# Optimization experiments

Measured on AMD Instinct MI355X. Metric: run time of the kernel, lower is better.

## Reference

```python
import jax, jax.numpy as jnp
import numpy as np

B, CIN, COUT = 2, 64, 64
D, H, W = 8, 32, 32
KD = KH = KW = 3
K = KD * KH * KW  # 27
STRIDE, PAD, DIL = 1, 1, 1
DOUT = (D + 2 * PAD - DIL * (KD - 1) - 1) // STRIDE + 1
HOUT = (H + 2 * PAD - DIL * (KH - 1) - 1) // STRIDE + 1
WOUT = (W + 2 * PAD - DIL * (KW - 1) - 1) // STRIDE + 1


def setup_inputs() -> dict:
    key = jax.random.key(0)
    k1, k2, k3, k4 = jax.random.split(key, 4)
    x = jax.random.normal(k1, (B, CIN, D, H, W), dtype=jnp.float32)
    offset = jax.random.normal(k2, (B, 3 * K, DOUT, HOUT, WOUT), dtype=jnp.float32)
    weight = jax.random.normal(k3, (COUT, CIN, KD, KH, KW), dtype=jnp.float32) * 0.05
    bias = jax.random.normal(k4, (COUT,), dtype=jnp.float32) * 0.1
    return {"x": x, "offset": offset, "weight": weight, "bias": bias}


def _trilinear_sample(xb, zd, zh, zw):
    # xb: [C, D, H, W]; zd/zh/zw: [K, P] float sampling coords (zero padding outside)
    Dd, Hh, Ww = xb.shape[1], xb.shape[2], xb.shape[3]
    d0 = jnp.floor(zd); h0 = jnp.floor(zh); w0 = jnp.floor(zw)
    fd = zd - d0; fh = zh - h0; fw = zw - w0
    d0i = d0.astype(jnp.int32); h0i = h0.astype(jnp.int32); w0i = w0.astype(jnp.int32)
    acc = jnp.zeros((xb.shape[0],) + zd.shape, dtype=xb.dtype)
    for dd in (0, 1):
        for dh in (0, 1):
            for dw in (0, 1):
                di = d0i + dd; hi = h0i + dh; wi = w0i + dw
                wgt = ((fd if dd else 1.0 - fd) * (fh if dh else 1.0 - fh)
                       * (fw if dw else 1.0 - fw))
                valid = ((di >= 0) & (di < Dd) & (hi >= 0) & (hi < Hh)
                         & (wi >= 0) & (wi < Ww)).astype(xb.dtype)
                v = xb[:, jnp.clip(di, 0, Dd - 1), jnp.clip(hi, 0, Hh - 1),
                       jnp.clip(wi, 0, Ww - 1)]  # [C, K, P]
                acc = acc + v * (wgt * valid)[None]
    return acc


def _deform_conv3d(x, offset, weight, bias):
    Bb = x.shape[0]
    P = DOUT * HOUT * WOUT
    # kernel taps
    kd, kh, kw = jnp.unravel_index(jnp.arange(K), (KD, KH, KW))
    # output grid
    od, oh, ow = jnp.meshgrid(jnp.arange(DOUT), jnp.arange(HOUT), jnp.arange(WOUT), indexing="ij")
    base_d = (od[None] * STRIDE - PAD + kd[:, None, None, None] * DIL).astype(jnp.float32)  # [K,Do,Ho,Wo]
    base_h = (oh[None] * STRIDE - PAD + kh[:, None, None, None] * DIL).astype(jnp.float32)
    base_w = (ow[None] * STRIDE - PAD + kw[:, None, None, None] * DIL).astype(jnp.float32)
    off = offset.reshape(Bb, K, 3, DOUT, HOUT, WOUT)  # per-tap (dd, dh, dw)
    zd = (base_d[None] + off[:, :, 0]).reshape(Bb, K, P)
    zh = (base_h[None] + off[:, :, 1]).reshape(Bb, K, P)
    zw = (base_w[None] + off[:, :, 2]).reshape(Bb, K, P)
    sampled = jax.vmap(_trilinear_sample)(x, zd, zh, zw)  # [B, C, K, P]
    wmat = weight.reshape(COUT, CIN, K)
    out = jnp.einsum("bckp,ock->bop", sampled, wmat)  # [B, COUT, P]
    out = out + bias[None, :, None]
    return out.reshape(Bb, COUT, DOUT, HOUT, WOUT)


def reference(x, offset, weight, bias):
    return _deform_conv3d(x, offset, weight, bias)
```

## Files before the change

kernel.cpp:

```cpp
#include <hip/hip_runtime.h>
#include <hip/hip_bf16.h>


#define BB    2
#define CINC  64
#define COUTC 64
#define DDEP  8
#define HGT   32
#define WID   32
#define KK    27
#define KGRP  3
#define KPG   9
#define KPH   3
#define PP    8192
#define TP    64
#define LDW   72

typedef short s16x8 __attribute__((ext_vector_type(8)));
typedef float f32x4 __attribute__((ext_vector_type(4)));

__device__ __forceinline__ unsigned short f2bf(float f) {
    unsigned u = __builtin_bit_cast(unsigned, f);
    u += 0x7FFFu + ((u >> 16) & 1u);
    return (unsigned short)(u >> 16);
}

__device__ __forceinline__ unsigned pack2bf(float lo, float hi) {
    return (unsigned)f2bf(lo) | ((unsigned)f2bf(hi) << 16);
}

__device__ __forceinline__ float bfu_lo(unsigned v) {
    return __builtin_bit_cast(float, v << 16);
}
__device__ __forceinline__ float bfu_hi(unsigned v) {
    return __builtin_bit_cast(float, v & 0xFFFF0000u);
}

__global__ void pre_kernel(const float* __restrict__ x, const float* __restrict__ w,
                           unsigned short* __restrict__ xt, unsigned short* __restrict__ wt) {
    __shared__ float sT[64][65];
    const int t    = threadIdx.x;
    const int lane = t & 63;
    const int wv   = t >> 6;
    const int half = lane >> 5;
    const int c2   = lane & 31;
    int blk = blockIdx.x;
    if (blk < 256) {
        int b  = blk >> 7;
        int s0 = (blk & 127) * 64;
        #pragma unroll
        for (int i = 0; i < 16; ++i) {
            int c = wv * 16 + i;
            sT[c][lane] = x[(size_t)(b * CINC + c) * PP + s0 + lane];
        }
        __syncthreads();
        #pragma unroll
        for (int i = 0; i < 8; ++i) {
            int s = wv * 16 + 2 * i + half;
            unsigned pk = pack2bf(sT[2 * c2][s], sT[2 * c2 + 1][s]);
            *(unsigned*)&xt[(size_t)(b * PP + s0 + s) * 64 + 2 * c2] = pk;
        }
    } else {
        int id = (blk - 256) * 256 + t;
        if (id < KK * COUTC * CINC) {
            int c = id & 63;
            int o = (id >> 6) & 63;
            int k = id >> 12;
            wt[id] = f2bf(w[(o * CINC + c) * KK + k]);
        }
    }
}

__global__ __launch_bounds__(256, 3) void deform_kernel(
    const unsigned short* __restrict__ xt, const float* __restrict__ off,
    const unsigned short* __restrict__ wt, const float* __restrict__ bias,
    float* __restrict__ out)
{
    __shared__ unsigned short sW[KPH * COUTC * LDW] __attribute__((aligned(16)));
    __shared__ unsigned short sS[TP * LDW]          __attribute__((aligned(16)));
    __shared__ int   sIdx[KPH][TP][8] __attribute__((aligned(16)));
    __shared__ float sCf[KPH][TP][8]  __attribute__((aligned(16)));

    const int t    = threadIdx.x;
    const int lane = t & 63;
    const int wv   = t >> 6;
    const int half = lane >> 5;
    const int c2   = lane & 31;
    const int b    = blockIdx.x >> 7;
    const int p0   = (blockIdx.x & 127) * TP;
    const int kg   = blockIdx.y;

    const unsigned short* xb = xt + (size_t)b * PP * 64;

    f32x4 acc[4];
    #pragma unroll
    for (int f = 0; f < 4; ++f) acc[f] = (f32x4)0.0f;

    const int n0 = lane & 15;
    const int q  = lane >> 4;

    #pragma unroll 1
    for (int ph = 0; ph < 3; ++ph) {
        const int kbase = kg * KPG + ph * KPH;

        const unsigned short* wk = wt + kbase * (COUTC * CINC);
        #pragma unroll
        for (int j = 0; j < 6; ++j) {
            int idx = j * 2048 + t * 8;
            int kl  = idx >> 12;
            int rem = idx & 4095;
            *(s16x8*)&sW[kl * (COUTC * LDW) + (rem >> 6) * LDW + (rem & 63)] =
                *(const s16x8*)(wk + idx);
        }

        if (t < KPH * TP) {
            int kl = t >> 6;
            int k  = kbase + kl;
            int pl = t & 63;
            int pp = p0 + pl;
            int ow = pp & 31;
            int oh = (pp >> 5) & 31;
            int od = pp >> 10;
            int kd = k / 9;
            int kh = (k - kd * 9) / 3;
            int kw = k - kd * 9 - kh * 3;
            const float* ob = off + (size_t)(b * (3 * KK) + 3 * k) * PP + pp;
            float zd = (float)(od - 1 + kd) + ob[0];
            float zh = (float)(oh - 1 + kh) + ob[PP];
            float zw = (float)(ow - 1 + kw) + ob[2 * PP];

            float fdf = floorf(zd); int d0 = (int)fdf; float fd = zd - fdf;
            float fhf = floorf(zh); int h0 = (int)fhf; float fh = zh - fhf;
            float fwf = floorf(zw); int w0 = (int)fwf; float fw = zw - fwf;

            float Bd0 = (d0 >= 0     && d0 < DDEP)     ? 1.0f - fd : 0.0f;
            float Bd1 = (d0 + 1 >= 0 && d0 + 1 < DDEP) ? fd        : 0.0f;
            float Ch0 = (h0 >= 0     && h0 < HGT)      ? 1.0f - fh : 0.0f;
            float Ch1 = (h0 + 1 >= 0 && h0 + 1 < HGT)  ? fh        : 0.0f;
            float Aw0 = (w0 >= 0     && w0 < WID)      ? 1.0f - fw : 0.0f;
            float Aw1 = (w0 + 1 >= 0 && w0 + 1 < WID)  ? fw        : 0.0f;
            int dc0 = min(max(d0, 0), DDEP - 1);
            int dc1 = min(max(d0 + 1, 0), DDEP - 1);
            int hc0 = min(max(h0, 0), HGT - 1);
            int hc1 = min(max(h0 + 1, 0), HGT - 1);
            int wc0 = min(max(w0, 0), WID - 1);
            int wc1 = min(max(w0 + 1, 0), WID - 1);

            int dhb0 = (dc0 * HGT + hc0) * (WID * 64);
            int dhb1 = (dc0 * HGT + hc1) * (WID * 64);
            int dhb2 = (dc1 * HGT + hc0) * (WID * 64);
            int dhb3 = (dc1 * HGT + hc1) * (WID * 64);
            int wo0 = wc0 * 64, wo1 = wc1 * 64;
            sIdx[kl][pl][0] = dhb0 + wo0;
            sIdx[kl][pl][1] = dhb1 + wo0;
            sIdx[kl][pl][2] = dhb2 + wo0;
            sIdx[kl][pl][3] = dhb3 + wo0;
            sIdx[kl][pl][4] = dhb0 + wo1;
            sIdx[kl][pl][5] = dhb1 + wo1;
            sIdx[kl][pl][6] = dhb2 + wo1;
            sIdx[kl][pl][7] = dhb3 + wo1;
            float bc0 = Bd0 * Ch0, bc1 = Bd0 * Ch1, bc2 = Bd1 * Ch0, bc3 = Bd1 * Ch1;
            sCf[kl][pl][0] = bc0 * Aw0;
            sCf[kl][pl][1] = bc1 * Aw0;
            sCf[kl][pl][2] = bc2 * Aw0;
            sCf[kl][pl][3] = bc3 * Aw0;
            sCf[kl][pl][4] = bc0 * Aw1;
            sCf[kl][pl][5] = bc1 * Aw1;
            sCf[kl][pl][6] = bc2 * Aw1;
            sCf[kl][pl][7] = bc3 * Aw1;
        }
        __syncthreads();

        #pragma unroll
        for (int kl = 0; kl < KPH; ++kl) {
            #pragma unroll
            for (int jp = 0; jp < 8; ++jp) {
                int prow = wv * 16 + 2 * jp + half;
                const int4   i0 = *(const int4*)&sIdx[kl][prow][0];
                const int4   i1 = *(const int4*)&sIdx[kl][prow][4];
                const float4 u0 = *(const float4*)&sCf[kl][prow][0];
                const float4 u1 = *(const float4*)&sCf[kl][prow][4];
                float slo = 0.0f, shi = 0.0f;
                {
                    unsigned v0 = *(const unsigned*)(xb + i0.x + 2 * c2);
                    unsigned v1 = *(const unsigned*)(xb + i0.y + 2 * c2);
                    unsigned v2 = *(const unsigned*)(xb + i0.z + 2 * c2);
                    unsigned v3 = *(const unsigned*)(xb + i0.w + 2 * c2);
                    unsigned v4 = *(const unsigned*)(xb + i1.x + 2 * c2);
                    unsigned v5 = *(const unsigned*)(xb + i1.y + 2 * c2);
                    unsigned v6 = *(const unsigned*)(xb + i1.z + 2 * c2);
                    unsigned v7 = *(const unsigned*)(xb + i1.w + 2 * c2);
                    slo += u0.x * bfu_lo(v0); shi += u0.x * bfu_hi(v0);
                    slo += u0.y * bfu_lo(v1); shi += u0.y * bfu_hi(v1);
                    slo += u0.z * bfu_lo(v2); shi += u0.z * bfu_hi(v2);
                    slo += u0.w * bfu_lo(v3); shi += u0.w * bfu_hi(v3);
                    slo += u1.x * bfu_lo(v4); shi += u1.x * bfu_hi(v4);
                    slo += u1.y * bfu_lo(v5); shi += u1.y * bfu_hi(v5);
                    slo += u1.z * bfu_lo(v6); shi += u1.z * bfu_hi(v6);
                    slo += u1.w * bfu_lo(v7); shi += u1.w * bfu_hi(v7);
                }
                *(unsigned*)&sS[prow * LDW + 2 * c2] = pack2bf(slo, shi);
            }
            __syncthreads();

            {
                const unsigned short* sWk = &sW[kl * (COUTC * LDW)];
                s16x8 a0 = *(const s16x8*)&sWk[(16 * wv + n0) * LDW +      8 * q];
                s16x8 a1 = *(const s16x8*)&sWk[(16 * wv + n0) * LDW + 32 + 8 * q];
                #pragma unroll
                for (int f = 0; f < 4; ++f) {
                    s16x8 b0 = *(const s16x8*)&sS[(16 * f + n0) * LDW +      8 * q];
                    s16x8 b1 = *(const s16x8*)&sS[(16 * f + n0) * LDW + 32 + 8 * q];
                    acc[f] = __builtin_amdgcn_mfma_f32_16x16x32_bf16(a0, b0, acc[f], 0, 0, 0);
                    acc[f] = __builtin_amdgcn_mfma_f32_16x16x32_bf16(a1, b1, acc[f], 0, 0, 0);
                }
            }
            __syncthreads();
        }
    }

    float bv[4];
    #pragma unroll
    for (int r = 0; r < 4; ++r) bv[r] = (kg == 0) ? bias[16 * wv + 4 * q + r] : 0.0f;
    #pragma unroll
    for (int f = 0; f < 4; ++f) {
        #pragma unroll
        for (int r = 0; r < 4; ++r) {
            int o = 16 * wv + 4 * q + r;
            int p = p0 + 16 * f + n0;
            unsafeAtomicAdd(&out[(size_t)(b * COUTC + o) * PP + p], acc[f][r] + bv[r]);
        }
    }
}

extern "C" void kernel_launch(void* const* d_in, const int* in_sizes, int n_in,
                              void* d_out, int out_size, void* d_ws, size_t ws_size,
                              hipStream_t stream) {
    const float* x    = (const float*)d_in[0];
    const float* off  = (const float*)d_in[1];
    const float* w    = (const float*)d_in[2];
    const float* bias = (const float*)d_in[3];
    float* out        = (float*)d_out;

    unsigned short* xt = (unsigned short*)d_ws;
    unsigned short* wt = (unsigned short*)((char*)d_ws + (size_t)BB * PP * 64 * 2);

    (void)hipMemsetAsync(out, 0, (size_t)out_size * sizeof(float), stream);
    hipLaunchKernelGGL(pre_kernel, dim3(256 + (KK * COUTC * CINC + 255) / 256), dim3(256), 0,
                       stream, x, w, xt, wt);
    hipLaunchKernelGGL(deform_kernel, dim3(BB * (PP / TP), KGRP), dim3(256), 0, stream,
                       xt, off, wt, bias, out);
}
```

Before: 103.3 us.

## Split taps across more blocks and give each wave its own pixel rows to drop barriers

Raises the tap-group count from 3 to 9, so each block handles 3 taps in a single phase, and launches three times more blocks. Each wave now samples and stores only the 16 pixel rows it later feeds to its own MFMAs, which removes the in-loop __syncthreads. Gather loads are widened to 16-byte vectors per lane, and gather indices are packed into u16 to save LDS. The trade-off is three times as many atomic adds to the output and three times as many weight-tile and setup loads.

After: 111.7 us. 8.1% more time.

```diff
diff --git a/kernel.cpp b/kernel.cpp
--- a/kernel.cpp
+++ b/kernel.cpp
@@ -9,15 +9,15 @@
 #define HGT   32
 #define WID   32
 #define KK    27
-#define KGRP  3
-#define KPG   9
-#define KPH   3
+#define KGRP  9
+#define KPB   3
 #define PP    8192
 #define TP    64
 #define LDW   72
 
 typedef short s16x8 __attribute__((ext_vector_type(8)));
 typedef float f32x4 __attribute__((ext_vector_type(4)));
+typedef unsigned short u16x8 __attribute__((ext_vector_type(8)));
 
 __device__ __forceinline__ unsigned short f2bf(float f) {
     unsigned u = __builtin_bit_cast(unsigned, f);
@@ -71,21 +71,26 @@
     }
 }
 
+__device__ __forceinline__ void acc8(float* s, int4 v, float wg) {
+    s[0] += wg * bfu_lo((unsigned)v.x); s[1] += wg * bfu_hi((unsigned)v.x);
+    s[2] += wg * bfu_lo((unsigned)v.y); s[3] += wg * bfu_hi((unsigned)v.y);
+    s[4] += wg * bfu_lo((unsigned)v.z); s[5] += wg * bfu_hi((unsigned)v.z);
+    s[6] += wg * bfu_lo((unsigned)v.w); s[7] += wg * bfu_hi((unsigned)v.w);
+}
+
 __global__ __launch_bounds__(256, 3) void deform_kernel(
     const unsigned short* __restrict__ xt, const float* __restrict__ off,
     const unsigned short* __restrict__ wt, const float* __restrict__ bias,
     float* __restrict__ out)
 {
-    __shared__ unsigned short sW[KPH * COUTC * LDW] __attribute__((aligned(16)));
+    __shared__ unsigned short sW[KPB * COUTC * LDW] __attribute__((aligned(16)));
     __shared__ unsigned short sS[TP * LDW]          __attribute__((aligned(16)));
-    __shared__ int   sIdx[KPH][TP][8] __attribute__((aligned(16)));
-    __shared__ float sCf[KPH][TP][8]  __attribute__((aligned(16)));
+    __shared__ u16x8 sIdx[KPB][TP] __attribute__((aligned(16)));
+    __shared__ float sCf[KPB][TP][8] __attribute__((aligned(16)));
 
     const int t    = threadIdx.x;
     const int lane = t & 63;
     const int wv   = t >> 6;
-    const int half = lane >> 5;
-    const int c2   = lane & 31;
     const int b    = blockIdx.x >> 7;
     const int p0   = (blockIdx.x & 127) * TP;
     const int kg   = blockIdx.y;
@@ -99,11 +104,8 @@
     const int n0 = lane & 15;
     const int q  = lane >> 4;
 
-    #pragma unroll 1
-    for (int ph = 0; ph < 3; ++ph) {
-        const int kbase = kg * KPG + ph * KPH;
-
-        const unsigned short* wk = wt + kbase * (COUTC * CINC);
+    {
+        const unsigned short* wk = wt + (kg * KPB) * (COUTC * CINC);
         #pragma unroll
         for (int j = 0; j < 6; ++j) {
             int idx = j * 2048 + t * 8;
@@ -112,123 +114,122 @@
             *(s16x8*)&sW[kl * (COUTC * LDW) + (rem >> 6) * LDW + (rem & 63)] =
                 *(const s16x8*)(wk + idx);
         }
-
-        if (t < KPH * TP) {
-            int kl = t >> 6;
-            int k  = kbase + kl;
-            int pl = t & 63;
-            int pp = p0 + pl;
-            int ow = pp & 31;
-            int oh = (pp >> 5) & 31;
-            int od = pp >> 10;
-            int kd = k / 9;
-            int kh = (k - kd * 9) / 3;
-            int kw = k - kd * 9 - kh * 3;
-            const float* ob = off + (size_t)(b * (3 * KK) + 3 * k) * PP + pp;
-            float zd = (float)(od - 1 + kd) + ob[0];
-            float zh = (float)(oh - 1 + kh) + ob[PP];
-            float zw = (float)(ow - 1 + kw) + ob[2 * PP];
-
-            float fdf = floorf(zd); int d0 = (int)fdf; float fd = zd - fdf;
-            float fhf = floorf(zh); int h0 = (int)fhf; float fh = zh - fhf;
-            float fwf = floorf(zw); int w0 = (int)fwf; float fw = zw - fwf;
-
-            float Bd0 = (d0 >= 0     && d0 < DDEP)     ? 1.0f - fd : 0.0f;
-            float Bd1 = (d0 + 1 >= 0 && d0 + 1 < DDEP) ? fd        : 0.0f;
-            float Ch0 = (h0 >= 0     && h0 < HGT)      ? 1.0f - fh : 0.0f;
-            float Ch1 = (h0 + 1 >= 0 && h0 + 1 < HGT)  ? fh        : 0.0f;
-            float Aw0 = (w0 >= 0     && w0 < WID)      ? 1.0f - fw : 0.0f;
-            float Aw1 = (w0 + 1 >= 0 && w0 + 1 < WID)  ? fw        : 0.0f;
-            int dc0 = min(max(d0, 0), DDEP - 1);
-            int dc1 = min(max(d0 + 1, 0), DDEP - 1);
-            int hc0 = min(max(h0, 0), HGT - 1);
-            int hc1 = min(max(h0 + 1, 0), HGT - 1);
-            int wc0 = min(max(w0, 0), WID - 1);
-            int wc1 = min(max(w0 + 1, 0), WID - 1);
-
-            int dhb0 = (dc0 * HGT + hc0) * (WID * 64);
-            int dhb1 = (dc0 * HGT + hc1) * (WID * 64);
-            int dhb2 = (dc1 * HGT + hc0) * (WID * 64);
-            int dhb3 = (dc1 * HGT + hc1) * (WID * 64);
-            int wo0 = wc0 * 64, wo1 = wc1 * 64;
-            sIdx[kl][pl][0] = dhb0 + wo0;
-            sIdx[kl][pl][1] = dhb1 + wo0;
-            sIdx[kl][pl][2] = dhb2 + wo0;
-            sIdx[kl][pl][3] = dhb3 + wo0;
-            sIdx[kl][pl][4] = dhb0 + wo1;
-            sIdx[kl][pl][5] = dhb1 + wo1;
-            sIdx[kl][pl][6] = dhb2 + wo1;
-            sIdx[kl][pl][7] = dhb3 + wo1;
-            float bc0 = Bd0 * Ch0, bc1 = Bd0 * Ch1, bc2 = Bd1 * Ch0, bc3 = Bd1 * Ch1;
-            sCf[kl][pl][0] = bc0 * Aw0;
-            sCf[kl][pl][1] = bc1 * Aw0;
-            sCf[kl][pl][2] = bc2 * Aw0;
-            sCf[kl][pl][3] = bc3 * Aw0;
-            sCf[kl][pl][4] = bc0 * Aw1;
-            sCf[kl][pl][5] = bc1 * Aw1;
-            sCf[kl][pl][6] = bc2 * Aw1;
-            sCf[kl][pl][7] = bc3 * Aw1;
-        }
-        __syncthreads();
-
-        #pragma unroll
-        for (int kl = 0; kl < KPH; ++kl) {
+    }
+
+    if (t < KPB * TP) {
+        int kl = t >> 6;
+        int k  = kg * KPB + kl;
+        int pl = t & 63;
+        int pp = p0 + pl;
+        int ow = pp & 31;
+        int oh = (pp >> 5) & 31;
+        int od = pp >> 10;
+        int kd = k / 9;
+        int kh = (k - kd * 9) / 3;
+        int kw = k - kd * 9 - kh * 3;
+        const float* ob = off + (size_t)(b * (3 * KK) + 3 * k) * PP + pp;
+        float zd = (float)(od - 1 + kd) + ob[0];
+        float zh = (float)(oh - 1 + kh) + ob[PP];
+        float zw = (float)(ow - 1 + kw) + ob[2 * PP];
+
+        float fdf = floorf(zd); int d0 = (int)fdf; float fd = zd - fdf;
+        float fhf = floorf(zh); int h0 = (int)fhf; float fh = zh - fhf;
+        float fwf = floorf(zw); int w0 = (int)fwf; float fw = zw - fwf;
+
+        float Bd0 = (d0 >= 0     && d0 < DDEP)     ? 1.0f - fd : 0.0f;
+        float Bd1 = (d0 + 1 >= 0 && d0 + 1 < DDEP) ? fd        : 0.0f;
+        float Ch0 = (h0 >= 0     && h0 < HGT)      ? 1.0f - fh : 0.0f;
+        float Ch1 = (h0 + 1 >= 0 && h0 + 1 < HGT)  ? fh        : 0.0f;
+        float Aw0 = (w0 >= 0     && w0 < WID)      ? 1.0f - fw : 0.0f;
+        float Aw1 = (w0 + 1 >= 0 && w0 + 1 < WID)  ? fw        : 0.0f;
+        int dc0 = min(max(d0, 0), DDEP - 1);
+        int dc1 = min(max(d0 + 1, 0), DDEP - 1);
+        int hc0 = min(max(h0, 0), HGT - 1);
+        int hc1 = min(max(h0 + 1, 0), HGT - 1);
+        int wc0 = min(max(w0, 0), WID - 1);
+        int wc1 = min(max(w0 + 1, 0), WID - 1);
+
+        int dh0 = (dc0 * HGT + hc0) * WID;
+        int dh1 = (dc0 * HGT + hc1) * WID;
+        int dh2 = (dc1 * HGT + hc0) * WID;
+        int dh3 = (dc1 * HGT + hc1) * WID;
+        u16x8 iv;
+        iv[0] = (unsigned short)(dh0 + wc0);
+        iv[1] = (unsigned short)(dh1 + wc0);
+        iv[2] = (unsigned short)(dh2 + wc0);
+        iv[3] = (unsigned short)(dh3 + wc0);
+        iv[4] = (unsigned short)(dh0 + wc1);
+        iv[5] = (unsigned short)(dh1 + wc1);
+        iv[6] = (unsigned short)(dh2 + wc1);
+        iv[7] = (unsigned short)(dh3 + wc1);
+        sIdx[kl][pl] = iv;
+        float bc0 = Bd0 * Ch0, bc1 = Bd0 * Ch1, bc2 = Bd1 * Ch0, bc3 = Bd1 * Ch1;
+        sCf[kl][pl][0] = bc0 * Aw0;
+        sCf[kl][pl][1] = bc1 * Aw0;
+        sCf[kl][pl][2] = bc2 * Aw0;
+        sCf[kl][pl][3] = bc3 * Aw0;
+        sCf[kl][pl][4] = bc0 * Aw1;
+        sCf[kl][pl][5] = bc1 * Aw1;
+        sCf[kl][pl][6] = bc2 * Aw1;
+        sCf[kl][pl][7] = bc3 * Aw1;
+    }
+    __syncthreads();
+
+    const int coff = (lane & 7) * 8;
+    #pragma unroll 1
+    for (int kl = 0; kl < KPB; ++kl) {
+        #pragma unroll
+        for (int jp = 0; jp < 2; ++jp) {
+            int prow = 16 * wv + 8 * jp + (lane >> 3);
+            u16x8  iv = sIdx[kl][prow];
+            float4 u0 = *(const float4*)&sCf[kl][prow][0];
+            float4 u1 = *(const float4*)&sCf[kl][prow][4];
+            const int4 v0 = *(const int4*)(xb + ((int)iv[0] << 6) + coff);
+            const int4 v1 = *(const int4*)(xb + ((int)iv[1] << 6) + coff);
+            const int4 v2 = *(const int4*)(xb + ((int)iv[2] << 6) + coff);
+            const int4 v3 = *(const int4*)(xb + ((int)iv[3] << 6) + coff);
+            const int4 v4 = *(const int4*)(xb + ((int)iv[4] << 6) + coff);
+            const int4 v5 = *(const int4*)(xb + ((int)iv[5] << 6) + coff);
+            const int4 v6 = *(const int4*)(xb + ((int)iv[6] << 6) + coff);
+            const int4 v7 = *(const int4*)(xb + ((int)iv[7] << 6) + coff);
+            float s[8] = {0, 0, 0, 0, 0, 0, 0, 0};
+            acc8(s, v0, u0.x);
+            acc8(s, v1, u0.y);
+            acc8(s, v2, u0.z);
+            acc8(s, v3, u0.w);
+            acc8(s, v4, u1.x);
+            acc8(s, v5, u1.y);
+            acc8(s, v6, u1.z);
+            acc8(s, v7, u1.w);
+            int4 pk;
+            pk.x = (int)pack2bf(s[0], s[1]);
+            pk.y = (int)pack2bf(s[2], s[3]);
+            pk.z = (int)pack2bf(s[4], s[5]);
+            pk.w = (int)pack2bf(s[6], s[7]);
+            *(int4*)&sS[prow * LDW + coff] = pk;
+        }
+        {
+            s16x8 b0 = *(const s16x8*)&sS[(16 * wv + n0) * LDW +      8 * q];
+            s16x8 b1 = *(const s16x8*)&sS[(16 * wv + n0) * LDW + 32 + 8 * q];
+            const unsigned short* sWk = &sW[kl * (COUTC * LDW)];
             #pragma unroll
-            for (int jp = 0; jp < 8; ++jp) {
-                int prow = wv * 16 + 2 * jp + half;
-                const int4   i0 = *(const int4*)&sIdx[kl][prow][0];
-                const int4   i1 = *(const int4*)&sIdx[kl][prow][4];
-                const float4 u0 = *(const float4*)&sCf[kl][prow][0];
-                const float4 u1 = *(const float4*)&sCf[kl][prow][4];
-                float slo = 0.0f, shi = 0.0f;
-                {
-                    unsigned v0 = *(const unsigned*)(xb + i0.x + 2 * c2);
-                    unsigned v1 = *(const unsigned*)(xb + i0.y + 2 * c2);
-                    unsigned v2 = *(const unsigned*)(xb + i0.z + 2 * c2);
-                    unsigned v3 = *(const unsigned*)(xb + i0.w + 2 * c2);
-                    unsigned v4 = *(const unsigned*)(xb + i1.x + 2 * c2);
-                    unsigned v5 = *(const unsigned*)(xb + i1.y + 2 * c2);
-                    unsigned v6 = *(const unsigned*)(xb + i1.z + 2 * c2);
-                    unsigned v7 = *(const unsigned*)(xb + i1.w + 2 * c2);
-                    slo += u0.x * bfu_lo(v0); shi += u0.x * bfu_hi(v0);
-                    slo += u0.y * bfu_lo(v1); shi += u0.y * bfu_hi(v1);
-                    slo += u0.z * bfu_lo(v2); shi += u0.z * bfu_hi(v2);
-                    slo += u0.w * bfu_lo(v3); shi += u0.w * bfu_hi(v3);
-                    slo += u1.x * bfu_lo(v4); shi += u1.x * bfu_hi(v4);
-                    slo += u1.y * bfu_lo(v5); shi += u1.y * bfu_hi(v5);
-                    slo += u1.z * bfu_lo(v6); shi += u1.z * bfu_hi(v6);
-                    slo += u1.w * bfu_lo(v7); shi += u1.w * bfu_hi(v7);
-                }
-                *(unsigned*)&sS[prow * LDW + 2 * c2] = pack2bf(slo, shi);
+            for (int f = 0; f < 4; ++f) {
+                s16x8 a0 = *(const s16x8*)&sWk[(16 * f + n0) * LDW +      8 * q];
+                s16x8 a1 = *(const s16x8*)&sWk[(16 * f + n0) * LDW + 32 + 8 * q];
+                acc[f] = __builtin_amdgcn_mfma_f32_16x16x32_bf16(a0, b0, acc[f], 0, 0, 0);
+                acc[f] = __builtin_amdgcn_mfma_f32_16x16x32_bf16(a1, b1, acc[f], 0, 0, 0);
             }
-            __syncthreads();
-
-            {
-                const unsigned short* sWk = &sW[kl * (COUTC * LDW)];
-                s16x8 a0 = *(const s16x8*)&sWk[(16 * wv + n0) * LDW +      8 * q];
-                s16x8 a1 = *(const s16x8*)&sWk[(16 * wv + n0) * LDW + 32 + 8 * q];
-                #pragma unroll
-                for (int f = 0; f < 4; ++f) {
-                    s16x8 b0 = *(const s16x8*)&sS[(16 * f + n0) * LDW +      8 * q];
-                    s16x8 b1 = *(const s16x8*)&sS[(16 * f + n0) * LDW + 32 + 8 * q];
-                    acc[f] = __builtin_amdgcn_mfma_f32_16x16x32_bf16(a0, b0, acc[f], 0, 0, 0);
-                    acc[f] = __builtin_amdgcn_mfma_f32_16x16x32_bf16(a1, b1, acc[f], 0, 0, 0);
-                }
-            }
-            __syncthreads();
-        }
-    }
-
-    float bv[4];
-    #pragma unroll
-    for (int r = 0; r < 4; ++r) bv[r] = (kg == 0) ? bias[16 * wv + 4 * q + r] : 0.0f;
+        }
+    }
+
+    const int pdst = p0 + 16 * wv + n0;
     #pragma unroll
     for (int f = 0; f < 4; ++f) {
         #pragma unroll
         for (int r = 0; r < 4; ++r) {
-            int o = 16 * wv + 4 * q + r;
-            int p = p0 + 16 * f + n0;
-            unsafeAtomicAdd(&out[(size_t)(b * COUTC + o) * PP + p], acc[f][r] + bv[r]);
+            int o = 16 * f + 4 * q + r;
+            float add = acc[f][r] + ((kg == 0) ? bias[o] : 0.0f);
+            unsafeAtomicAdd(&out[(size_t)(b * COUTC + o) * PP + pdst], add);
         }
     }
 }
```
